# Kernel tuning notes

Measured on AMD Instinct MI355X. Metric: run time of the kernel, lower is better.

The kernel has to match this reference:

```python
import jax, jax.numpy as jnp
import numpy as np

LN_EPS = 1e-5

def layer_norm(x, gamma, beta):
    mu = jnp.mean(x, axis=-1, keepdims=True)
    var = jnp.mean(jnp.square(x - mu), axis=-1, keepdims=True)
    return (x - mu) * jax.lax.rsqrt(var + LN_EPS) * gamma + beta

def setup_inputs() -> dict:
    key = jax.random.key(0)
    ks = jax.random.split(key, 10)
    B, C, N = 8, 256, 4096
    s = 1.0 / np.sqrt(C)
    inp = {
        "x": jax.random.normal(ks[0], (B, C, N), dtype=jnp.float32),
        "W_qkv": jax.random.uniform(ks[1], (C, C), jnp.float32, -s, s),            # Linear(dim, dim, bias=False)
        "W_mlp": jax.random.uniform(ks[2], (2 * C, 2 * C), jnp.float32, -0.5 * s, 0.5 * s),
        "b_mlp": jax.random.uniform(ks[3], (2 * C,), jnp.float32, -0.5 * s, 0.5 * s),
        "g1": jnp.ones((4 * C,), jnp.float32),
        "beta1": jnp.zeros((4 * C,), jnp.float32),
        "W_res": jax.random.uniform(ks[4], (C, 4 * C), jnp.float32, -0.25 * s, 0.25 * s),  # Linear(4*dim, dim, bias=False)
        "g2": jnp.ones((C,), jnp.float32),
        "beta2": jnp.zeros((C,), jnp.float32),
    }
    return inp

def reference(x, W_qkv, W_mlp, b_mlp, g1, beta1, W_res, g2, beta2):
    # x: (B, C, N) channels-first -> (B, N, C)
    NITER = 2  # niter_heads
    x = jnp.swapaxes(x, 1, 2)
    x = x @ W_qkv.T                                   # shared_qkv, (B, N, C)
    v = jax.lax.stop_gradient(x)                      # x.clone().detach()
    for _ in range(NITER):
        # first_context = x^T @ v : (B, C, C)
        ctx = jnp.einsum('bnc,bnd->bcd', x, v)
        out = jax.nn.softmax(x, axis=-1) @ ctx        # (B, N, C)
        cat1 = jnp.concatenate([out, v], axis=-1)     # (B, N, 2C)
        mlp = jax.nn.relu(cat1 @ W_mlp.T + b_mlp)     # (B, N, 2C)
        cat2 = jnp.concatenate([cat1, mlp], axis=-1)  # (B, N, 4C)
        # dropout layers are identity in eval mode
        v = layer_norm(cat2, g1, beta1) @ W_res.T + x # residual_mlp + skip
        v = layer_norm(x + v, g2, beta2)
    return jnp.swapaxes(v, 1, 2)                      # back to (B, C, N)
```

## Files before the change

### kernel.cpp

```cpp
#include <hip/hip_runtime.h>
#include <cstdint>
#include <cstddef>


using u16 = unsigned short;
using short8 = __attribute__((ext_vector_type(8))) short;
using bf16x8 = __attribute__((ext_vector_type(8))) __bf16;
using f32x4  = __attribute__((ext_vector_type(4))) float;
using i32x4  = __attribute__((ext_vector_type(4))) int;
using u16x4  = __attribute__((ext_vector_type(4))) u16;
using u16x8  = __attribute__((ext_vector_type(8))) u16;

__device__ __forceinline__ float b2f(u16 u) {
    union { unsigned u32; float f; } c; c.u32 = ((unsigned)u) << 16; return c.f;
}
__device__ __forceinline__ u16 f2b(float f) {
    union { float f; unsigned u; } c; c.f = f;
    unsigned r = c.u + 0x7FFFu + ((c.u >> 16) & 1u);
    return (u16)(r >> 16);
}
__device__ __forceinline__ void cvt(u16 a,  u16& o)   { o = a; }
__device__ __forceinline__ void cvt(float a, u16& o)  { o = f2b(a); }
__device__ __forceinline__ void cvt(float a, float& o){ o = a; }
__device__ __forceinline__ void cvt(u16 a,  float& o) { o = b2f(a); }

template<int MODE, int TRF>
__global__ __launch_bounds__(512)
void gemm_bt(const u16* __restrict__ A, const u16* __restrict__ A2,
             const u16* __restrict__ A3,
             int lda, int lda2, int lda3, int kSplit,
             const u16* __restrict__ B, int ldb, long strA, long strB,
             int statStride, int kChunk, int nKsplit,
             float* __restrict__ outF, u16* __restrict__ outB,
             long sOF, long sOB, int ldo,
             const u16* __restrict__ Xres,
             const float* __restrict__ bias,
             const float2* __restrict__ stats,
             const float* __restrict__ g, const float* __restrict__ be)
{
    __shared__ short lsA[128 * 72];
    __shared__ short lsB[128 * 72];

    const int bz    = blockIdx.z;
    const int batch = bz / nKsplit;
    const int ks    = bz - batch * nKsplit;
    const u16* Ab = A + (size_t)batch * strA;
    const u16* Bb = B + (size_t)batch * strB;
    const int colBase = blockIdx.x * 128;
    const int rowBase = blockIdx.y * 128;
    const int k0 = ks * kChunk;
    const int k1 = k0 + kChunk;

    const int t    = threadIdx.x;
    const int sRow = t >> 3;
    const int sKq  = (t & 7) << 3;

    const int lane = t & 63;
    const int w    = t >> 6;
    const int wr   = (w >> 1) * 32;
    const int wc   = (w & 1) * 64;
    const int mrow = lane & 15;
    const int q    = lane >> 4;

    float2 st0 = {0.f, 0.f}, st1 = {0.f, 0.f};
    if (TRF == 1) {
        const int sb = batch * statStride + rowBase;
        st0 = stats[sb + sRow];
        st1 = stats[sb + sRow + 64];
    }

    auto loadRaw = [&](int rloc, int kn) -> i32x4 {
        const int arow = rowBase + rloc + sRow;
        if (TRF == 2) {
            const u16* s; int ld; int kl;
            const int kc = kn + sKq;
            const int reg = kc >> 8;
            if (reg == 0)      { s = A;  ld = lda;  kl = kc; }
            else if (reg == 1) { s = A2; ld = lda2; kl = kc - 256; }
            else               { s = A3; ld = lda3; kl = kc - 512; }
            return *(const i32x4*)(s + (size_t)arow * ld + kl);
        } else if (TRF == 3) {
            const int kc = kn + sKq;
            if (kc < kSplit)
                return *(const i32x4*)(Ab + (size_t)arow * lda + kc);
            return *(const i32x4*)(A2 + (size_t)arow * lda2 + (kc - kSplit));
        }
        return *(const i32x4*)(Ab + (size_t)arow * lda + kn + sKq);
    };
    auto xform = [&](i32x4 raw, float2 st) -> i32x4 {
        if (TRF != 1) return raw;
        short8 h = __builtin_bit_cast(short8, raw);
        short8 o;
#pragma unroll
        for (int i = 0; i < 8; i++) {
            float v = b2f((u16)h[i]);
            v = __expf(v - st.x) * st.y;
            o[i] = (short)f2b(v);
        }
        return __builtin_bit_cast(i32x4, o);
    };

    const f32x4 fzero = {0.f, 0.f, 0.f, 0.f};
    f32x4 acc[2][4];
#pragma unroll
    for (int i = 0; i < 2; i++)
#pragma unroll
        for (int j = 0; j < 4; j++) acc[i][j] = fzero;

    const u16* pB0 = Bb + (size_t)(colBase + sRow) * ldb + sKq;
    const u16* pB1 = pB0 + (size_t)64 * ldb;

    i32x4 a0 = xform(loadRaw(0,  k0), st0);
    i32x4 a1 = xform(loadRaw(64, k0), st1);
    i32x4 b0 = *(const i32x4*)(pB0 + k0);
    i32x4 b1 = *(const i32x4*)(pB1 + k0);

    for (int kk = k0; kk < k1; kk += 64) {
        __syncthreads();
        *(i32x4*)&lsA[sRow * 72 + sKq]        = a0;
        *(i32x4*)&lsA[(sRow + 64) * 72 + sKq] = a1;
        *(i32x4*)&lsB[sRow * 72 + sKq]        = b0;
        *(i32x4*)&lsB[(sRow + 64) * 72 + sKq] = b1;
        __syncthreads();
        const int kn = kk + 64;
        if (kn < k1) {
            a0 = xform(loadRaw(0,  kn), st0);
            a1 = xform(loadRaw(64, kn), st1);
            b0 = *(const i32x4*)(pB0 + kn);
            b1 = *(const i32x4*)(pB1 + kn);
        }
#pragma unroll
        for (int h = 0; h < 2; h++) {
            bf16x8 af[2], bfr[4];
#pragma unroll
            for (int mi = 0; mi < 2; mi++)
                af[mi] = __builtin_bit_cast(bf16x8,
                    *(const short8*)&lsA[(wr + mi * 16 + mrow) * 72 + h * 32 + q * 8]);
#pragma unroll
            for (int ni = 0; ni < 4; ni++)
                bfr[ni] = __builtin_bit_cast(bf16x8,
                    *(const short8*)&lsB[(wc + ni * 16 + mrow) * 72 + h * 32 + q * 8]);
#pragma unroll
            for (int mi = 0; mi < 2; mi++)
#pragma unroll
                for (int ni = 0; ni < 4; ni++)
                    acc[mi][ni] = __builtin_amdgcn_mfma_f32_16x16x32_bf16(
                        af[mi], bfr[ni], acc[mi][ni], 0, 0, 0);
        }
    }

#pragma unroll
    for (int mi = 0; mi < 2; mi++) {
#pragma unroll
        for (int ni = 0; ni < 4; ni++) {
            const int col = colBase + wc + ni * 16 + mrow;
#pragma unroll
            for (int r = 0; r < 4; r++) {
                const int row = rowBase + wr + mi * 16 + q * 4 + r;
                float v = acc[mi][ni][r];
                if (MODE == 0) {
                    outB[(size_t)batch * sOB + (size_t)row * ldo + col] = f2b(v);
                } else if (MODE == 1) {
                    outF[((size_t)batch * nKsplit + ks) * sOF
                         + (size_t)row * ldo + col] = v;
                } else if (MODE == 3) {
                    v += bias[col];
                    v = v > 0.f ? v : 0.f;
                    outB[(size_t)row * ldo + col] = f2b(v);
                } else if (MODE == 4) {
                    const float2 ln = stats[row];
                    v = ln.y * (v - ln.x * g[col]) + be[col]
                        + 2.f * b2f(Xres[(size_t)row * 256 + col]);
                    outB[(size_t)row * ldo + col] = f2b(v);
                }
            }
        }
    }
}

template<typename TIN, typename TOUT>
__global__ __launch_bounds__(256)
void transpose_k(const TIN* __restrict__ in, TOUT* __restrict__ out,
                 int R, int Cc, long sIn, long sOut)
{
    __shared__ TOUT tile[32][33];
    const int b = blockIdx.z;
    const TIN* ib = in + (size_t)b * sIn;
    TOUT* ob = out + (size_t)b * sOut;
    const int c0 = blockIdx.x * 32, r0 = blockIdx.y * 32;
    const int tx = threadIdx.x & 31, ty = threadIdx.x >> 5;
#pragma unroll
    for (int i = 0; i < 32; i += 8)
        cvt(ib[(size_t)(r0 + ty + i) * Cc + c0 + tx], tile[ty + i][tx]);
    __syncthreads();
#pragma unroll
    for (int i = 0; i < 32; i += 8)
        ob[(size_t)(c0 + ty + i) * R + r0 + tx] = tile[tx][ty + i];
}

__global__ __launch_bounds__(256)
void smstats_k(const u16* __restrict__ Xb, float2* __restrict__ st)
{
    const int wave = threadIdx.x >> 6, lane = threadIdx.x & 63;
    const size_t row = (size_t)blockIdx.x * 4 + wave;
    const u16x4 xb = *(const u16x4*)(Xb + row * 256 + lane * 4);
    const float x0 = b2f(xb.x), x1 = b2f(xb.y), x2 = b2f(xb.z), x3 = b2f(xb.w);
    float m = fmaxf(fmaxf(x0, x1), fmaxf(x2, x3));
    for (int o = 32; o > 0; o >>= 1) m = fmaxf(m, __shfl_xor(m, o));
    float s = __expf(x0 - m) + __expf(x1 - m) + __expf(x2 - m) + __expf(x3 - m);
    for (int o = 32; o > 0; o >>= 1) s += __shfl_xor(s, o);
    if (lane == 0) st[row] = make_float2(m, 1.f / s);
}

__global__ __launch_bounds__(256)
void stats1024_k(const u16* __restrict__ OUT, const u16* __restrict__ V,
                 const u16* __restrict__ MLPo, float2* __restrict__ st)
{
    const int wave = threadIdx.x >> 6, lane = threadIdx.x & 63;
    const size_t row = (size_t)blockIdx.x * 4 + wave;
    const int c = lane * 16;
    const u16* src;
    if (c < 256)       src = OUT  + row * 256 + c;
    else if (c < 512)  src = V    + row * 256 + (c - 256);
    else               src = MLPo + row * 512 + (c - 512);
    short8 r0 = *(const short8*)(src);
    short8 r1 = *(const short8*)(src + 8);
    float s = 0.f, s2 = 0.f;
#pragma unroll
    for (int i = 0; i < 8; i++) {
        const float a = b2f((u16)r0[i]), b = b2f((u16)r1[i]);
        s += a + b; s2 += a * a + b * b;
    }
    for (int o = 32; o > 0; o >>= 1) { s += __shfl_xor(s, o); s2 += __shfl_xor(s2, o); }
    const float mean = s * (1.f / 1024.f);
    const float var  = s2 * (1.f / 1024.f) - mean * mean;
    if (lane == 0) st[row] = make_float2(mean, rsqrtf(var + 1e-5f));
}

template<typename OUTT, bool WRITE_VB>
__global__ __launch_bounds__(256)
void ln256t_k(const u16* __restrict__ Tb, const float* __restrict__ g,
              const float* __restrict__ be, u16* __restrict__ Vb,
              OUTT* __restrict__ outT)
{
    constexpr int STRIDE = (sizeof(OUTT) == 2) ? 266 : 261;
    __shared__ OUTT tile[32 * STRIDE];
    const int wid = threadIdx.x >> 6, lane = threadIdx.x & 63;
    const int bx = blockIdx.x;
    const size_t r0 = (size_t)bx * 32;
    const int b  = bx >> 7;
    const int n0 = (bx & 127) * 32;

#pragma unroll
    for (int j = 0; j < 8; j++) {
        const int lr = wid * 8 + j;
        const size_t row = r0 + lr;
        const u16x4 tb = *(const u16x4*)(Tb + row * 256 + lane * 4);
        const float x0 = b2f(tb.x), x1 = b2f(tb.y), x2 = b2f(tb.z), x3 = b2f(tb.w);
        float s  = x0 + x1 + x2 + x3;
        float s2 = x0 * x0 + x1 * x1 + x2 * x2 + x3 * x3;
        for (int o = 32; o > 0; o >>= 1) { s += __shfl_xor(s, o); s2 += __shfl_xor(s2, o); }
        const float mean = s * (1.f / 256.f);
        const float var  = s2 * (1.f / 256.f) - mean * mean;
        const float rstd = rsqrtf(var + 1e-5f);
        const int c = lane * 4;
        float4 ov = { (x0 - mean) * rstd * g[c + 0] + be[c + 0],
                      (x1 - mean) * rstd * g[c + 1] + be[c + 1],
                      (x2 - mean) * rstd * g[c + 2] + be[c + 2],
                      (x3 - mean) * rstd * g[c + 3] + be[c + 3] };
        if (WRITE_VB) {
            u16x4 vb = { f2b(ov.x), f2b(ov.y), f2b(ov.z), f2b(ov.w) };
            *(u16x4*)(Vb + row * 256 + c) = vb;
        }
        OUTT* tl = &tile[lr * STRIDE + c];
        cvt(ov.x, tl[0]); cvt(ov.y, tl[1]); cvt(ov.z, tl[2]); cvt(ov.w, tl[3]);
    }
    __syncthreads();

    const int c = threadIdx.x;
    OUTT* dst = outT + ((size_t)b * 256 + c) * 4096 + n0;
    if (sizeof(OUTT) == 2) {
#pragma unroll
        for (int k = 0; k < 4; k++) {
            u16x8 v;
#pragma unroll
            for (int i = 0; i < 8; i++) v[i] = *(const u16*)&tile[(k * 8 + i) * STRIDE + c];
            *(u16x8*)((u16*)dst + k * 8) = v;
        }
    } else {
#pragma unroll
        for (int k = 0; k < 8; k++) {
            float4 v;
            v.x = *(const float*)&tile[(k * 4 + 0) * STRIDE + c];
            v.y = *(const float*)&tile[(k * 4 + 1) * STRIDE + c];
            v.z = *(const float*)&tile[(k * 4 + 2) * STRIDE + c];
            v.w = *(const float*)&tile[(k * 4 + 3) * STRIDE + c];
            *(float4*)((float*)dst + k * 4) = v;
        }
    }
}

__global__ __launch_bounds__(256)
void ctxreduce_k(const float* __restrict__ ctxp, u16* __restrict__ ctxb)
{
    const int i = blockIdx.x * 256 + threadIdx.x;
    const int batch  = i >> 14;
    const int within = i & 16383;
    const float4* src = (const float4*)ctxp + (size_t)batch * 16 * 16384 + within;
    float4 s = {0.f, 0.f, 0.f, 0.f};
#pragma unroll
    for (int ks = 0; ks < 16; ks++) {
        const float4 v = src[(size_t)ks * 16384];
        s.x += v.x; s.y += v.y; s.z += v.z; s.w += v.w;
    }
    u16x4 o = { f2b(s.x), f2b(s.y), f2b(s.z), f2b(s.w) };
    ((u16x4*)ctxb)[i] = o;
}

__global__ __launch_bounds__(256)
void wconv_k(const float* __restrict__ Wq, const float* __restrict__ Wm,
             u16* __restrict__ oq, u16* __restrict__ om)
{
    const int i = blockIdx.x * 256 + threadIdx.x;
    const float* src; u16* dst; int j;
    if (i < 16384) { src = Wq; dst = oq; j = i; }
    else           { src = Wm; dst = om; j = i - 16384; }
    const float4 v = ((const float4*)src)[j];
    u16x4 o = { f2b(v.x), f2b(v.y), f2b(v.z), f2b(v.w) };
    ((u16x4*)dst)[j] = o;
}

__global__ __launch_bounds__(256)
void wresprep_k(const float* __restrict__ Wres, const float* __restrict__ g1,
                const float* __restrict__ be1, u16* __restrict__ Wr_b,
                float* __restrict__ sg, float* __restrict__ br)
{
    const int wv = threadIdx.x >> 6, lane = threadIdx.x & 63;
    const int row = blockIdx.x * 4 + wv;
    const float* src = Wres + (size_t)row * 1024;
    float s = 0.f, b = 0.f;
#pragma unroll
    for (int j = 0; j < 4; j++) {
        const int c = j * 256 + lane * 4;
        const float4 w  = *(const float4*)(src + c);
        const float4 gg = *(const float4*)(g1 + c);
        const float4 bb = *(const float4*)(be1 + c);
        const float4 wg = { w.x * gg.x, w.y * gg.y, w.z * gg.z, w.w * gg.w };
        u16x4 o = { f2b(wg.x), f2b(wg.y), f2b(wg.z), f2b(wg.w) };
        *(u16x4*)(Wr_b + (size_t)row * 1024 + c) = o;
        s += wg.x + wg.y + wg.z + wg.w;
        b += w.x * bb.x + w.y * bb.y + w.z * bb.z + w.w * bb.w;
    }
    for (int o = 32; o > 0; o >>= 1) { s += __shfl_xor(s, o); b += __shfl_xor(b, o); }
    if (lane == 0) { sg[row] = s; br[row] = b; }
}

extern "C" void kernel_launch(void* const* d_in, const int* in_sizes, int n_in,
                              void* d_out, int out_size, void* d_ws, size_t ws_size,
                              hipStream_t stream)
{
    (void)in_sizes; (void)n_in; (void)out_size; (void)ws_size;
    const float* x    = (const float*)d_in[0];
    const float* Wqkv = (const float*)d_in[1];
    const float* Wmlp = (const float*)d_in[2];
    const float* bmlp = (const float*)d_in[3];
    const float* g1   = (const float*)d_in[4];
    const float* be1  = (const float*)d_in[5];
    const float* Wres = (const float*)d_in[6];
    const float* g2   = (const float*)d_in[7];
    const float* be2  = (const float*)d_in[8];

    char* ws = (char*)d_ws;
    u16*    Xb   = (u16*)ws;    ws += (size_t)16777216;
    u16*    XT   = (u16*)ws;    ws += (size_t)16777216;
    u16*    Vb   = (u16*)ws;    ws += (size_t)16777216;
    u16*    VT2  = (u16*)ws;    ws += (size_t)16777216;
    u16*    OUT  = (u16*)ws;    ws += (size_t)16777216;
    u16*    MLPo = (u16*)ws;    ws += (size_t)33554432;
    u16*    Tb   = (u16*)ws;    ws += (size_t)16777216;
    float*  ctxp = (float*)ws;  ws += (size_t)33554432;
    u16*    ctxb = (u16*)ws;    ws += (size_t)1048576;
    float2* smst = (float2*)ws; ws += (size_t)262144;
    float2* lnst = (float2*)ws; ws += (size_t)262144;
    u16*    Wq_b = (u16*)ws;    ws += (size_t)131072;
    u16*    Wm_b = (u16*)ws;    ws += (size_t)524288;
    u16*    Wr_b = (u16*)ws;    ws += (size_t)524288;
    float*  sg   = (float*)ws;  ws += (size_t)1024;
    float*  br   = (float*)ws;  ws += (size_t)1024;
    u16*    xt   = MLPo;

    wconv_k<<<dim3(320), 256, 0, stream>>>(Wqkv, Wmlp, Wq_b, Wm_b);
    wresprep_k<<<dim3(64), 256, 0, stream>>>(Wres, g1, be1, Wr_b, sg, br);

    transpose_k<float, u16><<<dim3(128, 8, 8), 256, 0, stream>>>(
        x, xt, 256, 4096, 256L * 4096, 4096L * 256);

    gemm_bt<0, 0><<<dim3(2, 256, 1), 512, 0, stream>>>(
        xt, nullptr, nullptr, 256, 0, 0, 0, Wq_b, 256, 0, 0, 0, 256, 1,
        nullptr, Xb, 0, 0, 256, nullptr, nullptr, nullptr, nullptr, nullptr);

    transpose_k<u16, u16><<<dim3(8, 128, 8), 256, 0, stream>>>(
        Xb, XT, 4096, 256, 4096L * 256, 256L * 4096);

    const u16* VTcur = XT;
    const u16* Vcur  = Xb;

    for (int it = 0; it < 2; ++it) {
        smstats_k<<<dim3(8192), 256, 0, stream>>>(Xb, smst);

        gemm_bt<1, 0><<<dim3(2, 2, 128), 512, 0, stream>>>(
            VTcur, nullptr, nullptr, 4096, 0, 0, 0, XT, 4096,
            1048576, 1048576, 0, 256, 16,
            ctxp, nullptr, 65536, 0, 256, nullptr, nullptr, nullptr, nullptr, nullptr);
        ctxreduce_k<<<dim3(512), 256, 0, stream>>>(ctxp, ctxb);

        gemm_bt<0, 1><<<dim3(2, 32, 8), 512, 0, stream>>>(
            Xb, nullptr, nullptr, 256, 0, 0, 0, ctxb, 256,
            1048576, 65536, 4096, 256, 1,
            nullptr, OUT, 0, 1048576, 256, nullptr, nullptr, smst, nullptr, nullptr);

        gemm_bt<3, 3><<<dim3(4, 256, 1), 512, 0, stream>>>(
            OUT, Vcur, nullptr, 256, 256, 0, 256, Wm_b, 512, 0, 0, 0, 512, 1,
            nullptr, MLPo, 0, 0, 512, nullptr, bmlp, nullptr, nullptr, nullptr);

        stats1024_k<<<dim3(8192), 256, 0, stream>>>(OUT, Vcur, MLPo, lnst);

        gemm_bt<4, 2><<<dim3(2, 256, 1), 512, 0, stream>>>(
            OUT, Vcur, MLPo, 256, 256, 512, 0, Wr_b, 1024, 0, 0, 0, 1024, 1,
            nullptr, Tb, 0, 0, 256, Xb, nullptr, lnst, sg, br);

        if (it == 0) {
            ln256t_k<u16, true><<<dim3(1024), 256, 0, stream>>>(
                Tb, g2, be2, Vb, VT2);
            VTcur = VT2;
            Vcur  = Vb;
        } else {
            ln256t_k<float, false><<<dim3(1024), 256, 0, stream>>>(
                Tb, g2, be2, nullptr, (float*)d_out);
        }
    }
}
```

Baseline: 374.8 us.

## Load GEMM tiles directly into LDS with XOR swizzle; hoist softmax stats

Replaces register-staged global-to-LDS copies in the bf16 MFMA GEMM with global_load_lds direct transfers, swapping the padded LDS layout for an XOR-swizzled 64-wide layout to avoid bank conflicts. The loop now issues the loads and then syncs, so there is no register prefetch overlap for the non-exp paths. It also moves the softmax-stats kernel out of the two-iteration loop, because Xb does not change between iterations. Correctness depends on the direct-to-LDS write pattern (per wave, 512 shorts) lining up with the swizzled read addressing.

```diff
diff --git a/kernel.cpp b/kernel.cpp
--- a/kernel.cpp
+++ b/kernel.cpp
@@ -23,6 +23,12 @@
 __device__ __forceinline__ void cvt(float a, u16& o)  { o = f2b(a); }
 __device__ __forceinline__ void cvt(float a, float& o){ o = a; }
 __device__ __forceinline__ void cvt(u16 a,  float& o) { o = b2f(a); }
+
+__device__ __forceinline__ void glds16(const u16* g, short* l) {
+    __builtin_amdgcn_global_load_lds(
+        (const __attribute__((address_space(1))) void*)g,
+        (__attribute__((address_space(3))) void*)l, 16, 0, 0);
+}
 
 template<int MODE, int TRF>
 __global__ __launch_bounds__(512)
@@ -38,8 +44,8 @@
              const float2* __restrict__ stats,
              const float* __restrict__ g, const float* __restrict__ be)
 {
-    __shared__ short lsA[128 * 72];
-    __shared__ short lsB[128 * 72];
+    __shared__ short lsA[128 * 64];
+    __shared__ short lsB[128 * 64];
 
     const int bz    = blockIdx.z;
     const int batch = bz / nKsplit;
@@ -53,7 +59,8 @@
 
     const int t    = threadIdx.x;
     const int sRow = t >> 3;
-    const int sKq  = (t & 7) << 3;
+    const int sKl  = (t & 7) << 3;
+    const int sKg  = (((t & 7) ^ (sRow & 7)) << 3);
 
     const int lane = t & 63;
     const int w    = t >> 6;
@@ -62,6 +69,11 @@
     const int mrow = lane & 15;
     const int q    = lane >> 4;
 
+    short* ldA0 = &lsA[w * 512];
+    short* ldA1 = &lsA[4096 + w * 512];
+    short* ldB0 = &lsB[w * 512];
+    short* ldB1 = &lsB[4096 + w * 512];
+
     float2 st0 = {0.f, 0.f}, st1 = {0.f, 0.f};
     if (TRF == 1) {
         const int sb = batch * statStride + rowBase;
@@ -69,26 +81,21 @@
         st1 = stats[sb + sRow + 64];
     }
 
-    auto loadRaw = [&](int rloc, int kn) -> i32x4 {
+    auto aPtr = [&](int rloc, int kn) -> const u16* {
         const int arow = rowBase + rloc + sRow;
         if (TRF == 2) {
-            const u16* s; int ld; int kl;
-            const int kc = kn + sKq;
-            const int reg = kc >> 8;
-            if (reg == 0)      { s = A;  ld = lda;  kl = kc; }
-            else if (reg == 1) { s = A2; ld = lda2; kl = kc - 256; }
-            else               { s = A3; ld = lda3; kl = kc - 512; }
-            return *(const i32x4*)(s + (size_t)arow * ld + kl);
+            if (kn < 256)      return A  + (size_t)arow * lda  + kn + sKg;
+            else if (kn < 512) return A2 + (size_t)arow * lda2 + (kn - 256) + sKg;
+            else               return A3 + (size_t)arow * lda3 + (kn - 512) + sKg;
         } else if (TRF == 3) {
-            const int kc = kn + sKq;
-            if (kc < kSplit)
-                return *(const i32x4*)(Ab + (size_t)arow * lda + kc);
-            return *(const i32x4*)(A2 + (size_t)arow * lda2 + (kc - kSplit));
-        }
-        return *(const i32x4*)(Ab + (size_t)arow * lda + kn + sKq);
+            if (kn < kSplit)   return Ab + (size_t)arow * lda + kn + sKg;
+            return A2 + (size_t)arow * lda2 + (kn - kSplit) + sKg;
+        }
+        return Ab + (size_t)arow * lda + kn + sKg;
     };
-    auto xform = [&](i32x4 raw, float2 st) -> i32x4 {
-        if (TRF != 1) return raw;
+    auto loadX = [&](int rloc, int kn, float2 st) -> i32x4 {
+        const int arow = rowBase + rloc + sRow;
+        i32x4 raw = *(const i32x4*)(Ab + (size_t)arow * lda + kn + sKg);
         short8 h = __builtin_bit_cast(short8, raw);
         short8 o;
 #pragma unroll
@@ -107,39 +114,55 @@
 #pragma unroll
         for (int j = 0; j < 4; j++) acc[i][j] = fzero;
 
-    const u16* pB0 = Bb + (size_t)(colBase + sRow) * ldb + sKq;
+    const u16* pB0 = Bb + (size_t)(colBase + sRow) * ldb + sKg;
     const u16* pB1 = pB0 + (size_t)64 * ldb;
-
-    i32x4 a0 = xform(loadRaw(0,  k0), st0);
-    i32x4 a1 = xform(loadRaw(64, k0), st1);
-    i32x4 b0 = *(const i32x4*)(pB0 + k0);
-    i32x4 b1 = *(const i32x4*)(pB1 + k0);
+    const u16* pA0 = nullptr; const u16* pA1 = nullptr;
+    if (TRF == 0) {
+        pA0 = Ab + (size_t)(rowBase + sRow) * lda + sKg;
+        pA1 = pA0 + (size_t)64 * lda;
+    }
+
+    const int rsw = mrow & 7;
+    const int kc0 = (((0 * 4 + q) ^ rsw) << 3);
+    const int kc1 = (((1 * 4 + q) ^ rsw) << 3);
+
+    i32x4 a0, a1;
+    if (TRF == 1) {
+        a0 = loadX(0,  k0, st0);
+        a1 = loadX(64, k0, st1);
+    }
 
     for (int kk = k0; kk < k1; kk += 64) {
-        __syncthreads();
-        *(i32x4*)&lsA[sRow * 72 + sKq]        = a0;
-        *(i32x4*)&lsA[(sRow + 64) * 72 + sKq] = a1;
-        *(i32x4*)&lsB[sRow * 72 + sKq]        = b0;
-        *(i32x4*)&lsB[(sRow + 64) * 72 + sKq] = b1;
+        if (TRF == 1) {
+            *(i32x4*)&lsA[sRow * 64 + sKl]        = a0;
+            *(i32x4*)&lsA[(sRow + 64) * 64 + sKl] = a1;
+        } else if (TRF == 0) {
+            glds16(pA0 + kk, ldA0);
+            glds16(pA1 + kk, ldA1);
+        } else {
+            glds16(aPtr(0,  kk), ldA0);
+            glds16(aPtr(64, kk), ldA1);
+        }
+        glds16(pB0 + kk, ldB0);
+        glds16(pB1 + kk, ldB1);
         __syncthreads();
         const int kn = kk + 64;
-        if (kn < k1) {
-            a0 = xform(loadRaw(0,  kn), st0);
-            a1 = xform(loadRaw(64, kn), st1);
-            b0 = *(const i32x4*)(pB0 + kn);
-            b1 = *(const i32x4*)(pB1 + kn);
+        if (TRF == 1 && kn < k1) {
+            a0 = loadX(0,  kn, st0);
+            a1 = loadX(64, kn, st1);
         }
 #pragma unroll
         for (int h = 0; h < 2; h++) {
+            const int kc = h ? kc1 : kc0;
             bf16x8 af[2], bfr[4];
 #pragma unroll
             for (int mi = 0; mi < 2; mi++)
                 af[mi] = __builtin_bit_cast(bf16x8,
-                    *(const short8*)&lsA[(wr + mi * 16 + mrow) * 72 + h * 32 + q * 8]);
+                    *(const short8*)&lsA[(wr + mi * 16 + mrow) * 64 + kc]);
 #pragma unroll
             for (int ni = 0; ni < 4; ni++)
                 bfr[ni] = __builtin_bit_cast(bf16x8,
-                    *(const short8*)&lsB[(wc + ni * 16 + mrow) * 72 + h * 32 + q * 8]);
+                    *(const short8*)&lsB[(wc + ni * 16 + mrow) * 64 + kc]);
 #pragma unroll
             for (int mi = 0; mi < 2; mi++)
 #pragma unroll
@@ -147,6 +170,7 @@
                     acc[mi][ni] = __builtin_amdgcn_mfma_f32_16x16x32_bf16(
                         af[mi], bfr[ni], acc[mi][ni], 0, 0, 0);
         }
+        __syncthreads();
     }
 
 #pragma unroll
@@ -399,6 +423,8 @@
         xt, nullptr, nullptr, 256, 0, 0, 0, Wq_b, 256, 0, 0, 0, 256, 1,
         nullptr, Xb, 0, 0, 256, nullptr, nullptr, nullptr, nullptr, nullptr);
 
+    smstats_k<<<dim3(8192), 256, 0, stream>>>(Xb, smst);
+
     transpose_k<u16, u16><<<dim3(8, 128, 8), 256, 0, stream>>>(
         Xb, XT, 4096, 256, 4096L * 256, 256L * 4096);
 
@@ -406,8 +432,6 @@
     const u16* Vcur  = Xb;
 
     for (int it = 0; it < 2; ++it) {
-        smstats_k<<<dim3(8192), 256, 0, stream>>>(Xb, smst);
-
         gemm_bt<1, 0><<<dim3(2, 2, 128), 512, 0, stream>>>(
             VTcur, nullptr, nullptr, 4096, 0, 0, 0, XT, 4096,
             1048576, 1048576, 0, 256, 16,
```

Result: faster. 362.7 us (-3.2%).
